# Kernel optimization log

Hardware: AMD Instinct MI355X
Metric: run time of the kernel (lower is better)

## Reference

```python
import jax, jax.numpy as jnp
import numpy as np
from jax import lax

VOL = 96 ** 3        # AvgPool3d(kernel_size=96) pooling volume
GAMMA = 0.2          # cam_threshold (gamma default in update())
NUM_CLASSES = 14


def conv3d_same(x, w, b):
    # Conv3d(kernel_size=3, padding=1), NCDHW layout
    y = lax.conv_general_dilated(
        x, w, window_strides=(1, 1, 1),
        padding=((1, 1), (1, 1), (1, 1)),
        dimension_numbers=('NCDHW', 'OIDHW', 'NCDHW'))
    return y + b[None, :, None, None, None]


def maxpool3d_2(x):
    return lax.reduce_window(x, -jnp.inf, lax.max,
                             (1, 1, 2, 2, 2), (1, 1, 2, 2, 2), 'VALID')


def dom_classifier(x, c1w, c1b, c2w, c2b, lw, lb):
    x = jax.nn.relu(maxpool3d_2(conv3d_same(x, c1w, c1b)))   # [N,128,2,2,2]
    x = jax.nn.relu(maxpool3d_2(conv3d_same(x, c2w, c2b)))   # [N,64,1,1,1]
    x = x.reshape(x.shape[0], -1)                            # [N,64]
    return x @ lw.T + lb                                     # [N,1]


def get_cam(feature):
    # torch.autograd.functional.jacobian of AvgPool3d(96) on a [1,C,96,96,96]
    # input is analytically delta(c,c')/96^3 at every voxel; the subsequent
    # mean over spatial dims keeps eye(C)/96^3. Same math, closed form.
    n, c = feature.shape[:2]
    weight = jnp.broadcast_to(jnp.eye(c, dtype=feature.dtype) / VOL, (n, c, c))
    # einsum(weight, feature, 'n cls ch, n ch h w d -> n cls h w d')
    cam = jnp.einsum('nkc,ncxyz->nkxyz', weight, feature)
    return jax.nn.relu(cam)


def reference(feature, masks, dom_feat, conv1_w, conv1_b, conv2_w, conv2_b,
              lin_w, lin_b):
    cam = get_cam(feature)[:, 1:]                 # drop background class
    cam = cam * (cam > GAMMA)                     # cam *= cam > threshold
    pseudo = jnp.argmax(cam, axis=1, keepdims=True).astype(masks.dtype)
    updated_masks = masks + pseudo * (masks == 0)
    dom_logits = dom_classifier(dom_feat, conv1_w, conv1_b,
                                conv2_w, conv2_b, lin_w, lin_b)
    return cam, pseudo, updated_masks, dom_logits


def setup_inputs() -> dict:
    key = jax.random.key(0)
    ks = jax.random.split(key, 8)
    return {
        'feature': jax.random.normal(ks[0], (2, NUM_CLASSES, 96, 96, 96), jnp.float32),
        'masks': jax.random.randint(ks[1], (2, 1, 96, 96, 96), 0, NUM_CLASSES, jnp.int32),
        'dom_feat': jax.random.normal(ks[2], (2, 256, 4, 4, 4), jnp.float32),
        'conv1_w': jax.random.normal(ks[3], (128, 256, 3, 3, 3), jnp.float32) * 0.05,
        'conv1_b': jnp.zeros((128,), jnp.float32),
        'conv2_w': jax.random.normal(ks[4], (64, 128, 3, 3, 3), jnp.float32) * 0.05,
        'conv2_b': jnp.zeros((64,), jnp.float32),
        'lin_w': jax.random.normal(ks[5], (1, 64), jnp.float32) * 0.05,
        'lin_b': jnp.zeros((1,), jnp.float32),
    }
```

## Files before the change

kernel.cpp:

```cpp
#include <hip/hip_runtime.h>

#define VOXELS   884736
#define OUT_CAM  0
#define OUT_PSE  23003136
#define OUT_MSK  24772608
#define OUT_LOG  26542080

#define WS_WT 0
#define WS_P  884736
#define WS_H1 1769472

typedef float  f32x4 __attribute__((ext_vector_type(4)));
typedef int    i32x4 __attribute__((ext_vector_type(4)));

__global__ __launch_bounds__(256, 4) void k_cam(const float* __restrict__ feat,
                                                const int*   __restrict__ masks,
                                                float* __restrict__ out) {
  int bx = blockIdx.x;
  int n  = bx >= 864;
  int q  = (bx - n * 864) * 256 + threadIdx.x;
  int v  = q * 4;
  const float scale = 1.0f / 884736.0f;

  f32x4 f[13];
#pragma unroll
  for (int k = 0; k < 13; ++k)
    f[k] = *(const f32x4*)(feat + (size_t)(n * 14 + 1 + k) * VOXELS + v);
  i32x4 m = *(const i32x4*)(masks + (size_t)n * VOXELS + v);
  asm volatile(""
               : "+v"(f[0]), "+v"(f[1]), "+v"(f[2]), "+v"(f[3]), "+v"(f[4]),
                 "+v"(f[5]), "+v"(f[6]), "+v"(f[7]), "+v"(f[8]), "+v"(f[9]),
                 "+v"(f[10]), "+v"(f[11]), "+v"(f[12]), "+v"(m));

  f32x4 best = {0, 0, 0, 0};
  i32x4 bi = {0, 0, 0, 0};
#pragma unroll
  for (int k = 0; k < 13; ++k) {
    f32x4 t = f[k] * scale;
    t.x = (t.x > 0.2f) ? t.x : 0.0f;
    t.y = (t.y > 0.2f) ? t.y : 0.0f;
    t.z = (t.z > 0.2f) ? t.z : 0.0f;
    t.w = (t.w > 0.2f) ? t.w : 0.0f;
    __builtin_nontemporal_store(t, (f32x4*)(out + OUT_CAM + (size_t)(n * 13 + k) * VOXELS + v));
    if (k == 0) {
      best = t;
    } else {
      if (t.x > best.x) { best.x = t.x; bi.x = k; }
      if (t.y > best.y) { best.y = t.y; bi.y = k; }
      if (t.z > best.z) { best.z = t.z; bi.z = k; }
      if (t.w > best.w) { best.w = t.w; bi.w = k; }
    }
  }
  f32x4 ps = {(float)bi.x, (float)bi.y, (float)bi.z, (float)bi.w};
  f32x4 um;
  um.x = (m.x == 0) ? ps.x : (float)m.x;
  um.y = (m.y == 0) ? ps.y : (float)m.y;
  um.z = (m.z == 0) ? ps.z : (float)m.z;
  um.w = (m.w == 0) ? ps.w : (float)m.w;
  __builtin_nontemporal_store(ps, (f32x4*)(out + OUT_PSE + (size_t)n * VOXELS + v));
  __builtin_nontemporal_store(um, (f32x4*)(out + OUT_MSK + (size_t)n * VOXELS + v));
}

__global__ __launch_bounds__(256) void k_trans(const float* __restrict__ w1,
                                               float* __restrict__ wt,
                                               float* __restrict__ logits) {
  __shared__ float s[6912];
  int r0 = blockIdx.x * 256;
  int tid = threadIdx.x;
  if (blockIdx.x == 0 && tid < 2) logits[tid] = 0.0f;
  for (int i = tid; i < 1728; i += 256)
    *(f32x4*)&s[i * 4] = *(const f32x4*)&w1[(size_t)r0 * 27 + i * 4];
  __syncthreads();
#pragma unroll
  for (int tap = 0; tap < 27; ++tap)
    wt[tap * 32768 + r0 + tid] = s[tid * 27 + tap];
}

#define WSTRIDE 68
__global__ __launch_bounds__(256) void k_conv1(const float* __restrict__ dom,
                                               const float* __restrict__ wt,
                                               float* __restrict__ P) {
  __shared__ float Wl[128 * WSTRIDE];
  __shared__ float Xl[128 * 64];
  int bx = blockIdx.x;
  int och = bx & 1;
  int ich = (bx >> 1) & 1;
  int rest = bx >> 2;
  int tap = rest % 27;
  int n = rest / 27;
  int kd = tap / 9 - 1, kh = (tap % 9) / 3 - 1, kw = tap % 3 - 1;
  int I0 = ich * 128, O0 = och * 64;
  int tid = threadIdx.x;

  for (int i = tid; i < 2048; i += 256) {
    int oc = i >> 5, k4 = (i & 31) << 2;
    f32x4 rd = *(const f32x4*)&wt[(size_t)(tap * 128 + O0 + oc) * 256 + I0 + k4];
    Wl[(k4 + 0) * WSTRIDE + oc] = rd.x;
    Wl[(k4 + 1) * WSTRIDE + oc] = rd.y;
    Wl[(k4 + 2) * WSTRIDE + oc] = rd.z;
    Wl[(k4 + 3) * WSTRIDE + oc] = rd.w;
  }
  for (int i = tid; i < 8192; i += 256) {
    int kk = i >> 6, pos = i & 63;
    int d = pos >> 4, h = (pos >> 2) & 3, w = pos & 3;
    int sd = d + kd, sh = h + kh, sw = w + kw;
    bool ok = ((unsigned)sd < 4u) && ((unsigned)sh < 4u) && ((unsigned)sw < 4u);
    Xl[i] = ok ? dom[((n * 256 + I0 + kk) << 6) + sd * 16 + sh * 4 + sw] : 0.0f;
  }
  __syncthreads();

  int to = tid >> 4, tp = tid & 15;
  f32x4 acc0 = {0, 0, 0, 0}, acc1 = {0, 0, 0, 0}, acc2 = {0, 0, 0, 0}, acc3 = {0, 0, 0, 0};
#pragma unroll 4
  for (int kk = 0; kk < 128; ++kk) {
    f32x4 a = *(f32x4*)&Wl[kk * WSTRIDE + to * 4];
    f32x4 b = *(f32x4*)&Xl[kk * 64 + tp * 4];
    acc0 += a.x * b;
    acc1 += a.y * b;
    acc2 += a.z * b;
    acc3 += a.w * b;
  }
  float* pb = P + (size_t)((tap * 2 + ich) * 2 + n) * 8192 + (O0 + to * 4) * 64 + tp * 4;
  *(f32x4*)(pb +   0) = acc0;
  *(f32x4*)(pb +  64) = acc1;
  *(f32x4*)(pb + 128) = acc2;
  *(f32x4*)(pb + 192) = acc3;
}

__global__ __launch_bounds__(256) void k_pool1(const float* __restrict__ P,
                                               const float* __restrict__ b1,
                                               float* __restrict__ h1) {
  __shared__ float s[256];
  int n = blockIdx.x >> 7, oc = blockIdx.x & 127;
  int tid = threadIdx.x, pos = tid & 63, sg = tid >> 6;
  float sum = 0.0f;
#pragma unroll
  for (int j = 0; j < 14; ++j) {
    int sl = sg + j * 4;
    if (sl < 54) sum += P[((size_t)(sl * 2 + n) * 128 + oc) * 64 + pos];
  }
  s[tid] = sum;
  __syncthreads();
  if (tid < 64) {
    float tot = b1[oc] + s[pos] + s[64 + pos] + s[128 + pos] + s[192 + pos];
    s[pos] = tot;
  }
  __syncthreads();
  if (tid < 8) {
    int pd = tid >> 2, ph = (tid >> 1) & 1, pw = tid & 1;
    float m = -3.402823466e38f;
#pragma unroll
    for (int dd = 0; dd < 2; ++dd)
#pragma unroll
      for (int hh = 0; hh < 2; ++hh)
#pragma unroll
        for (int ww = 0; ww < 2; ++ww)
          m = fmaxf(m, s[(pd * 2 + dd) * 16 + (ph * 2 + hh) * 4 + (pw * 2 + ww)]);
    h1[(n * 128 + oc) * 8 + tid] = fmaxf(m, 0.0f);
  }
}

__global__ __launch_bounds__(64) void k_conv2(const float* __restrict__ h1,
                                              const float* __restrict__ w2,
                                              const float* __restrict__ b2,
                                              const float* __restrict__ lw,
                                              const float* __restrict__ lb,
                                              float* __restrict__ logits) {
  __shared__ float hl[1024];
  __shared__ float wl[3456];
  __shared__ float red[64];
  int n = blockIdx.x >> 6, oc = blockIdx.x & 63;
  int tid = threadIdx.x;
  for (int i = tid; i < 1024; i += 64) hl[i] = h1[n * 1024 + i];
  for (int i = tid; i < 3456; i += 64) wl[i] = w2[oc * 3456 + i];
  __syncthreads();
  int p = tid & 7, g = tid >> 3;
  int d = p >> 2, h = (p >> 1) & 1, w = p & 1;
  float acc = 0.0f;
  for (int ic = g * 16; ic < g * 16 + 16; ++ic) {
#pragma unroll
    for (int a = 0; a < 2; ++a)
#pragma unroll
      for (int b = 0; b < 2; ++b)
#pragma unroll
        for (int c = 0; c < 2; ++c) {
          int tapi = (a - d + 1) * 9 + (b - h + 1) * 3 + (c - w + 1);
          acc += hl[ic * 8 + a * 4 + b * 2 + c] * wl[ic * 27 + tapi];
        }
  }
  red[tid] = acc;
  __syncthreads();
  if (tid == 0) {
    float mx = -3.402823466e38f;
#pragma unroll
    for (int pp = 0; pp < 8; ++pp) {
      float sv = b2[oc];
#pragma unroll
      for (int gg = 0; gg < 8; ++gg) sv += red[gg * 8 + pp];
      mx = fmaxf(mx, sv);
    }
    float h2v = fmaxf(mx, 0.0f);
    atomicAdd(&logits[n], h2v * lw[oc]);
    if (oc == 0) atomicAdd(&logits[n], lb[0]);
  }
}

extern "C" void kernel_launch(void* const* d_in, const int* in_sizes, int n_in,
                              void* d_out, int out_size, void* d_ws, size_t ws_size,
                              hipStream_t stream) {
  const float* feat  = (const float*)d_in[0];
  const int*   masks = (const int*)  d_in[1];
  const float* dom   = (const float*)d_in[2];
  const float* w1    = (const float*)d_in[3];
  const float* b1    = (const float*)d_in[4];
  const float* w2    = (const float*)d_in[5];
  const float* b2    = (const float*)d_in[6];
  const float* lw    = (const float*)d_in[7];
  const float* lb    = (const float*)d_in[8];
  float* out = (float*)d_out;
  float* ws  = (float*)d_ws;
  float* wt  = ws + WS_WT;
  float* P   = ws + WS_P;
  float* h1  = ws + WS_H1;
  float* logits = out + OUT_LOG;

  k_trans<<<128, 256, 0, stream>>>(w1, wt, logits);
  k_conv1<<<216, 256, 0, stream>>>(dom, wt, P);
  k_pool1<<<256, 256, 0, stream>>>(P, b1, h1);
  k_conv2<<<128, 64, 0, stream>>>(h1, w2, b2, lw, lb, logits);
  k_cam<<<1728, 256, 0, stream>>>(feat, masks, out);
}
```

Baseline: 245.2 us.

## Split cam class channels across four thread groups with shared-memory argmax merge

Measured after the change: 244.1 us. About the same (-0.5%).

```diff
diff --git a/kernel.cpp b/kernel.cpp
--- a/kernel.cpp
+++ b/kernel.cpp
@@ -13,52 +13,79 @@
 typedef float  f32x4 __attribute__((ext_vector_type(4)));
 typedef int    i32x4 __attribute__((ext_vector_type(4)));
 
-__global__ __launch_bounds__(256, 4) void k_cam(const float* __restrict__ feat,
-                                                const int*   __restrict__ masks,
-                                                float* __restrict__ out) {
+#define CMP(tv, kk)                                             \
+  {                                                             \
+    if (tv.x > best.x) { best.x = tv.x; bi.x = (kk); }          \
+    if (tv.y > best.y) { best.y = tv.y; bi.y = (kk); }          \
+    if (tv.z > best.z) { best.z = tv.z; bi.z = (kk); }          \
+    if (tv.w > best.w) { best.w = tv.w; bi.w = (kk); }          \
+  }
+
+__global__ __launch_bounds__(1024) void k_cam(const float* __restrict__ feat,
+                                              const int*   __restrict__ masks,
+                                              float* __restrict__ out) {
+  __shared__ f32x4 sbv[3][256];
+  __shared__ i32x4 sbi[3][256];
   int bx = blockIdx.x;
   int n  = bx >= 864;
-  int q  = (bx - n * 864) * 256 + threadIdx.x;
+  int t  = threadIdx.x & 255;
+  int g  = threadIdx.x >> 8;
+  int q  = (bx - n * 864) * 256 + t;
   int v  = q * 4;
   const float scale = 1.0f / 884736.0f;
-
-  f32x4 f[13];
-#pragma unroll
-  for (int k = 0; k < 13; ++k)
-    f[k] = *(const f32x4*)(feat + (size_t)(n * 14 + 1 + k) * VOXELS + v);
-  i32x4 m = *(const i32x4*)(masks + (size_t)n * VOXELS + v);
-  asm volatile(""
-               : "+v"(f[0]), "+v"(f[1]), "+v"(f[2]), "+v"(f[3]), "+v"(f[4]),
-                 "+v"(f[5]), "+v"(f[6]), "+v"(f[7]), "+v"(f[8]), "+v"(f[9]),
-                 "+v"(f[10]), "+v"(f[11]), "+v"(f[12]), "+v"(m));
-
-  f32x4 best = {0, 0, 0, 0};
-  i32x4 bi = {0, 0, 0, 0};
-#pragma unroll
-  for (int k = 0; k < 13; ++k) {
-    f32x4 t = f[k] * scale;
-    t.x = (t.x > 0.2f) ? t.x : 0.0f;
-    t.y = (t.y > 0.2f) ? t.y : 0.0f;
-    t.z = (t.z > 0.2f) ? t.z : 0.0f;
-    t.w = (t.w > 0.2f) ? t.w : 0.0f;
-    __builtin_nontemporal_store(t, (f32x4*)(out + OUT_CAM + (size_t)(n * 13 + k) * VOXELS + v));
-    if (k == 0) {
-      best = t;
-    } else {
-      if (t.x > best.x) { best.x = t.x; bi.x = k; }
-      if (t.y > best.y) { best.y = t.y; bi.y = k; }
-      if (t.z > best.z) { best.z = t.z; bi.z = k; }
-      if (t.w > best.w) { best.w = t.w; bi.w = k; }
+  int k0 = g * 3;
+
+  i32x4 m = {0, 0, 0, 0};
+  if (g == 0) m = *(const i32x4*)(masks + (size_t)n * VOXELS + v);
+
+  const float* fb = feat + (size_t)(n * 14 + 1) * VOXELS + v;
+  f32x4 f0 = *(const f32x4*)(fb + (size_t)(k0 + 0) * VOXELS);
+  f32x4 f1 = *(const f32x4*)(fb + (size_t)(k0 + 1) * VOXELS);
+  f32x4 f2 = *(const f32x4*)(fb + (size_t)(k0 + 2) * VOXELS);
+  f32x4 f3 = *(const f32x4*)(fb + (size_t)(k0 + 3) * VOXELS);
+
+  f32x4 t0 = f0 * scale, t1 = f1 * scale, t2 = f2 * scale, t3 = f3 * scale;
+  t0.x = (t0.x > 0.2f) ? t0.x : 0.0f;  t0.y = (t0.y > 0.2f) ? t0.y : 0.0f;
+  t0.z = (t0.z > 0.2f) ? t0.z : 0.0f;  t0.w = (t0.w > 0.2f) ? t0.w : 0.0f;
+  t1.x = (t1.x > 0.2f) ? t1.x : 0.0f;  t1.y = (t1.y > 0.2f) ? t1.y : 0.0f;
+  t1.z = (t1.z > 0.2f) ? t1.z : 0.0f;  t1.w = (t1.w > 0.2f) ? t1.w : 0.0f;
+  t2.x = (t2.x > 0.2f) ? t2.x : 0.0f;  t2.y = (t2.y > 0.2f) ? t2.y : 0.0f;
+  t2.z = (t2.z > 0.2f) ? t2.z : 0.0f;  t2.w = (t2.w > 0.2f) ? t2.w : 0.0f;
+  t3.x = (t3.x > 0.2f) ? t3.x : 0.0f;  t3.y = (t3.y > 0.2f) ? t3.y : 0.0f;
+  t3.z = (t3.z > 0.2f) ? t3.z : 0.0f;  t3.w = (t3.w > 0.2f) ? t3.w : 0.0f;
+
+  float* cb = out + OUT_CAM + (size_t)(n * 13) * VOXELS + v;
+  if (g == 0)
+    __builtin_nontemporal_store(t0, (f32x4*)(cb + (size_t)(k0 + 0) * VOXELS));
+  __builtin_nontemporal_store(t1, (f32x4*)(cb + (size_t)(k0 + 1) * VOXELS));
+  __builtin_nontemporal_store(t2, (f32x4*)(cb + (size_t)(k0 + 2) * VOXELS));
+  __builtin_nontemporal_store(t3, (f32x4*)(cb + (size_t)(k0 + 3) * VOXELS));
+
+  f32x4 best = t0;
+  i32x4 bi = {k0, k0, k0, k0};
+  CMP(t1, k0 + 1); CMP(t2, k0 + 2); CMP(t3, k0 + 3);
+
+  if (g) { sbv[g - 1][t] = best; sbi[g - 1][t] = bi; }
+  __syncthreads();
+  if (g == 0) {
+#pragma unroll
+    for (int gg = 0; gg < 3; ++gg) {
+      f32x4 pb = sbv[gg][t];
+      i32x4 pi = sbi[gg][t];
+      if (pb.x > best.x) { best.x = pb.x; bi.x = pi.x; }
+      if (pb.y > best.y) { best.y = pb.y; bi.y = pi.y; }
+      if (pb.z > best.z) { best.z = pb.z; bi.z = pi.z; }
+      if (pb.w > best.w) { best.w = pb.w; bi.w = pi.w; }
     }
-  }
-  f32x4 ps = {(float)bi.x, (float)bi.y, (float)bi.z, (float)bi.w};
-  f32x4 um;
-  um.x = (m.x == 0) ? ps.x : (float)m.x;
-  um.y = (m.y == 0) ? ps.y : (float)m.y;
-  um.z = (m.z == 0) ? ps.z : (float)m.z;
-  um.w = (m.w == 0) ? ps.w : (float)m.w;
-  __builtin_nontemporal_store(ps, (f32x4*)(out + OUT_PSE + (size_t)n * VOXELS + v));
-  __builtin_nontemporal_store(um, (f32x4*)(out + OUT_MSK + (size_t)n * VOXELS + v));
+    f32x4 ps = {(float)bi.x, (float)bi.y, (float)bi.z, (float)bi.w};
+    f32x4 um;
+    um.x = (m.x == 0) ? ps.x : (float)m.x;
+    um.y = (m.y == 0) ? ps.y : (float)m.y;
+    um.z = (m.z == 0) ? ps.z : (float)m.z;
+    um.w = (m.w == 0) ? ps.w : (float)m.w;
+    __builtin_nontemporal_store(ps, (f32x4*)(out + OUT_PSE + (size_t)n * VOXELS + v));
+    __builtin_nontemporal_store(um, (f32x4*)(out + OUT_MSK + (size_t)n * VOXELS + v));
+  }
 }
 
 __global__ __launch_bounds__(256) void k_trans(const float* __restrict__ w1,
@@ -228,5 +255,5 @@
   k_conv1<<<216, 256, 0, stream>>>(dom, wt, P);
   k_pool1<<<256, 256, 0, stream>>>(P, b1, h1);
   k_conv2<<<128, 64, 0, stream>>>(h1, w2, b2, lw, lb, logits);
-  k_cam<<<1728, 256, 0, stream>>>(feat, masks, out);
-}
+  k_cam<<<1728, 1024, 0, stream>>>(feat, masks, out);
+}
```
